# Optimization experiments

Measured on AMD Instinct MI355X. Metric: run time of the kernel, lower is better.

Reference implementation:

```python
import jax, jax.numpy as jnp
import numpy as np

B, N, E, H = 2, 2048, 2048, 16
D = E // H  # head_dim = 128


def setup_inputs() -> dict:
    key = jax.random.key(0)
    k1, k2, k3, k4 = jax.random.split(key, 4)
    x = jax.random.normal(k1, (B, N, E), dtype=jnp.float32)
    Wq = jax.random.normal(k2, (E, E), dtype=jnp.float32) * 0.02
    Wkv = jax.random.normal(k3, (2 * E, E), dtype=jnp.float32) * 0.02
    Wout = jax.random.normal(k4, (E, E), dtype=jnp.float32) * 0.02
    return {"x": x, "Wq": Wq, "Wkv": Wkv, "Wout": Wout}


def reference(x, Wq, Wkv, Wout):
    # projections (torch Linear: y = x @ W.T)
    q = x @ Wq.T                      # [b, n, e]
    kv = x @ Wkv.T                    # [b, n, 2e]
    k, v = jnp.split(kv, 2, axis=-1)  # each [b, n, e]

    def split_heads(t):
        return t.reshape(B, N, H, D).transpose(0, 2, 1, 3)  # [b, h, n, d]

    q, k, v = split_heads(q), split_heads(k), split_heads(v)

    scale = D ** -0.5
    sim = jnp.einsum('bhid,bhjd->bhij', q * scale, k)  # [b, h, n, n]

    # causal mask: triu(j - i + 1) masks strictly-future positions
    mask_value = -jnp.finfo(sim.dtype).max
    causal_mask = jnp.triu(jnp.ones((N, N), dtype=bool), k=1)
    sim = jnp.where(causal_mask, mask_value, sim)

    attn = jax.nn.softmax(sim, axis=-1)
    out = jnp.einsum('bhij,bhjd->bhid', attn, v)  # [b, h, n, d]
    out = out.transpose(0, 2, 1, 3).reshape(B, N, E)
    return out @ Wout.T
```

## Files before the change

### kernel.cpp

```cpp
#include <hip/hip_runtime.h>


typedef __bf16 bf16;
typedef bf16 bf16x2 __attribute__((ext_vector_type(2)));
typedef bf16 bf16x4 __attribute__((ext_vector_type(4)));
typedef bf16 bf16x8 __attribute__((ext_vector_type(8)));
typedef float f32x4 __attribute__((ext_vector_type(4)));
typedef float f32x16 __attribute__((ext_vector_type(16)));

typedef const __attribute__((address_space(1))) void cg_void;
typedef __attribute__((address_space(3))) void lds_void;

#define MFMA16(a, b, c) __builtin_amdgcn_mfma_f32_16x16x32_bf16((a), (b), (c), 0, 0, 0)
#define MFMA32(a, b, c) __builtin_amdgcn_mfma_f32_32x32x16_bf16((a), (b), (c), 0, 0, 0)

__device__ __forceinline__ void async_load16(const bf16* g, bf16* l) {
  __builtin_amdgcn_global_load_lds((cg_void*)g, (lds_void*)l, 16, 0, 0);
}

__global__ __launch_bounds__(256) void cast_all_kernel(
    const float* __restrict__ x, const float* __restrict__ wq,
    const float* __restrict__ wkv, const float* __restrict__ wout,
    bf16* __restrict__ xb, bf16* __restrict__ wqkvb, bf16* __restrict__ woutb) {
  long i = (long)blockIdx.x * 256 + threadIdx.x;
  const float* src; bf16* dst; long off;
  if (i < 1048576)      { src = x;    dst = xb;            off = i; }
  else if (i < 2621440) { src = wq;   dst = wqkvb;         off = i - 1048576;
                          if (off >= 524288) { src = wkv; dst = wqkvb + 4194304; off -= 524288; } }
  else                  { src = wout; dst = woutb;         off = i - 2621440; }
  float4 f0 = ((const float4*)src)[2 * off];
  float4 f1 = ((const float4*)src)[2 * off + 1];
  bf16x8 o;
  o[0] = (bf16)f0.x; o[1] = (bf16)f0.y; o[2] = (bf16)f0.z; o[3] = (bf16)f0.w;
  o[4] = (bf16)f1.x; o[5] = (bf16)f1.y; o[6] = (bf16)f1.z; o[7] = (bf16)f1.w;
  ((bf16x8*)dst)[off] = o;
}

#define STAGE_A(bufi, h, tt) do {                              \
    const bf16* g_ = Ag + (h) * 262144 + (tt) * 64;            \
    bf16* d_ = ldsA + (bufi) * 16384 + (h) * 8192;             \
    async_load16(g_, d_);                                      \
    async_load16(g_ + 131072, d_ + 4096);                      \
  } while (0)
#define STAGE_B(bufi, h, tt) do {                              \
    const bf16* g_ = Bg + (h) * 262144 + (tt) * 64;            \
    bf16* d_ = ldsB + (bufi) * 16384 + (h) * 8192;             \
    async_load16(g_, d_);                                      \
    async_load16(g_ + 131072, d_ + 4096);                      \
  } while (0)

__global__ __launch_bounds__(512, 2)
void gemm_qkv_8phase(const bf16* __restrict__ A, const bf16* __restrict__ B,
                     bf16* __restrict__ qk, bf16* __restrict__ vt) {
  __shared__ __attribute__((aligned(16))) bf16 sm[2][2][256][64];
  const int tid = threadIdx.x;
  const int lane = tid & 63;
  const int wid = tid >> 6;
  const int quad = lane >> 4, l15 = lane & 15;
  const int wr = wid >> 2, wc = wid & 3;

  const int lb = (blockIdx.x & 7) * 48 + (blockIdx.x >> 3);
  const int bn = lb % 24, bm = lb / 24;
  const int m0 = bm * 256, n0 = bn * 256;

  const int srow = tid >> 3;
  const int kswz8 = ((tid & 7) ^ (srow & 7)) * 8;
  const bf16* Ag = A + (size_t)(m0 + srow) * 2048 + kswz8;
  const bf16* Bg = B + (size_t)(n0 + srow) * 2048 + kswz8;
  bf16* ldsA = &sm[0][0][0][0] + tid * 8;
  bf16* ldsB = &sm[1][0][0][0] + tid * 8;

  f32x4 acc[8][4];
#pragma unroll
  for (int i = 0; i < 8; ++i)
#pragma unroll
    for (int j = 0; j < 4; ++j) acc[i][j] = {0.f, 0.f, 0.f, 0.f};

  const int r7 = l15 & 7;
  const int c0 = (quad ^ r7) * 8;
  const int c1 = ((4 + quad) ^ r7) * 8;
  const int arow = (wr * 128 + l15) * 64;
  const int brow = (wc * 64 + l15) * 64;

  STAGE_A(0, 0, 0); STAGE_A(0, 1, 0); STAGE_B(0, 0, 0); STAGE_B(0, 1, 0);
  STAGE_A(1, 0, 1);
  asm volatile("s_waitcnt vmcnt(2)" ::: "memory");
  __builtin_amdgcn_s_barrier();

  for (int t = 0; t < 32; ++t) {
    const int cur = t & 1;
    const bf16* as = &sm[0][0][0][0] + cur * 16384;
    const bf16* bs = &sm[1][0][0][0] + cur * 16384;
#pragma unroll
    for (int q = 0; q < 4; ++q) {
      const int fi = (q >> 1) * 4, fj = (q & 1) * 2;
      bf16x8 af[4][2], bfr[2][2];
#pragma unroll
      for (int i = 0; i < 4; ++i) {
        af[i][0] = *(const bf16x8*)(as + arow + (fi + i) * 1024 + c0);
        af[i][1] = *(const bf16x8*)(as + arow + (fi + i) * 1024 + c1);
      }
#pragma unroll
      for (int j = 0; j < 2; ++j) {
        bfr[j][0] = *(const bf16x8*)(bs + brow + (fj + j) * 1024 + c0);
        bfr[j][1] = *(const bf16x8*)(bs + brow + (fj + j) * 1024 + c1);
      }
      if (t < 31) {
        const int nb = 1 - cur;
        if (q == 0) STAGE_A(nb, 1, t + 1);
        if (q == 1) STAGE_B(nb, 0, t + 1);
        if (q == 2) STAGE_B(nb, 1, t + 1);
      }
      __builtin_amdgcn_s_barrier();
      asm volatile("s_waitcnt lgkmcnt(0)" ::: "memory");
      __builtin_amdgcn_s_setprio(1);
#pragma unroll
      for (int ks = 0; ks < 2; ++ks)
#pragma unroll
        for (int i = 0; i < 4; ++i)
#pragma unroll
          for (int j = 0; j < 2; ++j)
            acc[fi + i][fj + j] = MFMA16(af[i][ks], bfr[j][ks], acc[fi + i][fj + j]);
      __builtin_amdgcn_s_setprio(0);
      __builtin_amdgcn_s_barrier();
    }
    if (t < 30) {
      STAGE_A(cur, 0, t + 2);
      asm volatile("s_waitcnt vmcnt(2)" ::: "memory");
      __builtin_amdgcn_s_barrier();
    } else if (t == 30) {
      asm volatile("s_waitcnt vmcnt(0)" ::: "memory");
      __builtin_amdgcn_s_barrier();
    }
  }

  if (n0 < 4096) {
#pragma unroll
    for (int i = 0; i < 8; ++i)
#pragma unroll
      for (int r = 0; r < 4; ++r) {
        const size_t base = (size_t)(m0 + wr * 128 + i * 16 + quad * 4 + r) * 4096
                          + n0 + wc * 64 + l15;
#pragma unroll
        for (int j = 0; j < 4; ++j) qk[base + j * 16] = (bf16)acc[i][j][r];
      }
  } else {
    __syncthreads();
    bf16* T = &sm[0][0][0][0];
#pragma unroll
    for (int i = 0; i < 8; ++i)
#pragma unroll
      for (int r = 0; r < 4; ++r) {
        const int nl = wr * 128 + i * 16 + quad * 4 + r;
#pragma unroll
        for (int j = 0; j < 4; ++j) {
          const int fl = wc * 64 + j * 16 + l15;
          T[fl * 256 + ((((nl >> 3) ^ (fl & 31)) << 3) | (nl & 7))] = (bf16)acc[i][j][r];
        }
      }
    __syncthreads();
    const int f0g = n0 - 4096, nb0 = m0 & 2047, b = m0 >> 11;
#pragma unroll
    for (int c = 0; c < 16; ++c) {
      const int idx = c * 512 + tid;
      const int fl = idx >> 5, nb = idx & 31;
      bf16x8 o = *(const bf16x8*)(T + fl * 256 + ((nb ^ (fl & 31)) << 3));
      *(bf16x8*)(vt + (size_t)(b * 2048 + f0g + fl) * 2048 + nb0 + nb * 8) = o;
    }
  }
}

__global__ __launch_bounds__(256, 4)
void gemm_out_kernel(const bf16* __restrict__ A, const bf16* __restrict__ B,
                     float* __restrict__ C, int K, int NN) {
  __shared__ __attribute__((aligned(16))) bf16 smem[8192];
  bf16* As = smem;
  bf16* Bs = smem + 4096;
  const int tid = threadIdx.x;
  const int wave = tid >> 6, lane = tid & 63;
  const int quad = lane >> 4, l15 = lane & 15;
  const int m0 = blockIdx.y * 128, n0 = blockIdx.x * 128;
  const int wm = (wave >> 1) * 64, wn = (wave & 1) * 64;

  f32x4 acc[4][4];
#pragma unroll
  for (int i = 0; i < 4; ++i)
#pragma unroll
    for (int j = 0; j < 4; ++j) acc[i][j] = {0.f, 0.f, 0.f, 0.f};

  const int srow = tid >> 2;
  const int scol = (tid & 3) * 8;
  const bf16* aG = A + (size_t)(m0 + srow) * K + scol;
  const bf16* bG = B + (size_t)(n0 + srow) * K + scol;
  bf16* aL = As + srow * 32 + scol;
  bf16* bL = Bs + srow * 32 + scol;
  const size_t gstep = (size_t)64 * K;

  for (int kt = 0; kt < K; kt += 32) {
    __syncthreads();
    async_load16(aG, aL);
    async_load16(aG + gstep, aL + 64 * 32);
    async_load16(bG, bL);
    async_load16(bG + gstep, bL + 64 * 32);
    aG += 32; bG += 32;
    __syncthreads();

    bf16x8 af[4], bfr[4];
#pragma unroll
    for (int i = 0; i < 4; ++i)
      af[i] = *(const bf16x8*)(As + (wm + i * 16 + l15) * 32 + quad * 8);
#pragma unroll
    for (int j = 0; j < 4; ++j)
      bfr[j] = *(const bf16x8*)(Bs + (wn + j * 16 + l15) * 32 + quad * 8);
#pragma unroll
    for (int i = 0; i < 4; ++i)
#pragma unroll
      for (int j = 0; j < 4; ++j) acc[i][j] = MFMA16(af[i], bfr[j], acc[i][j]);
  }

#pragma unroll
  for (int i = 0; i < 4; ++i) {
#pragma unroll
    for (int r = 0; r < 4; ++r) {
      int row = m0 + wm + i * 16 + quad * 4 + r;
      size_t base = (size_t)row * NN + n0 + wn + l15;
#pragma unroll
      for (int j = 0; j < 4; ++j) C[base + j * 16] = (float)acc[i][j][r];
    }
  }
}

__global__ __launch_bounds__(256, 2)
void attn_kernel(const bf16* __restrict__ qk, const bf16* __restrict__ vt,
                 bf16* __restrict__ yb) {
  constexpr int NSEQ = 2048, E = 2048, QKS = 4096;
  __shared__ __attribute__((aligned(16))) bf16 Ks[2][64 * 128];
  __shared__ __attribute__((aligned(16))) bf16 Vs[2][128 * 64];
  const int tid = threadIdx.x;
  const int wave = tid >> 6, lane = tid & 63;
  const int l31 = lane & 31, half = lane >> 5;
  const int id = blockIdx.x;
  const int slot = (id >> 5) & 15;
  const int bh = (id & 7) | (((id >> 3) & 3) << 3);
  const int b = bh >> 4, h = bh & 15;
  const int qt = (slot < 8) ? slot : 23 - slot;
  const float c1 = 0.08838834764831845f * 1.44269504088896f;

  const int krow_s = tid >> 4, kch_s = tid & 15;
  const int vrow_s = tid >> 3, vch_s = tid & 7;
  const bf16* kg = qk + (size_t)(b * NSEQ) * QKS + 2048 + h * 128;
  const bf16* vg = vt + (size_t)b * E * NSEQ + (size_t)(h * 128) * NSEQ;

  const int diag = 2 * qt + (wave >> 1);
  const int ktmax = 2 * qt + 1;

  {
    bf16* kdst = Ks[0] + tid * 8;
    bf16* vdst = Vs[0] + tid * 8;
#pragma unroll
    for (int p = 0; p < 4; ++p) {
      int r = p * 16 + krow_s;
      async_load16(kg + (size_t)r * QKS + (kch_s ^ (r & 7)) * 8, kdst + p * 2048);
    }
#pragma unroll
    for (int p = 0; p < 4; ++p) {
      int r = p * 32 + vrow_s;
      async_load16(vg + (size_t)r * NSEQ + (vch_s ^ (r & 7)) * 8, vdst + p * 2048);
    }
  }

  const int qrow = qt * 128 + wave * 32 + l31;
  bf16x8 qf[8];
  {
    const bf16* qp = qk + (size_t)(b * NSEQ + qrow) * QKS + h * 128 + half * 8;
#pragma unroll
    for (int k8 = 0; k8 < 8; ++k8) qf[k8] = *(const bf16x8*)(qp + k8 * 16);
  }

  float m = -3.0e38f, l = 0.f;
  f32x16 accO[4];
#pragma unroll
  for (int md = 0; md < 4; ++md)
#pragma unroll
    for (int r = 0; r < 16; ++r) accO[md][r] = 0.f;

  union PU { unsigned u; bf16x2 h; };
  union FU { bf16x8 v; unsigned u[4]; };

  for (int kt = 0; kt <= ktmax; ++kt) {
    const int cur = kt & 1;
    __syncthreads();

    if (kt < ktmax) {
      const int nxt = kt + 1;
      bf16* kdst = Ks[1 - cur] + tid * 8;
      bf16* vdst = Vs[1 - cur] + tid * 8;
#pragma unroll
      for (int p = 0; p < 4; ++p) {
        int r = p * 16 + krow_s;
        async_load16(kg + (size_t)(nxt * 64 + r) * QKS + (kch_s ^ (r & 7)) * 8, kdst + p * 2048);
      }
#pragma unroll
      for (int p = 0; p < 4; ++p) {
        int r = p * 32 + vrow_s;
        async_load16(vg + (size_t)r * NSEQ + nxt * 64 + (vch_s ^ (r & 7)) * 8, vdst + p * 2048);
      }
    }

    if (kt > diag) continue;

    const bf16* ks = Ks[cur];
    const bf16* vs = Vs[cur];

    f32x16 st[2];
#pragma unroll
    for (int mt = 0; mt < 2; ++mt)
#pragma unroll
      for (int r = 0; r < 16; ++r) st[mt][r] = 0.f;
#pragma unroll
    for (int k8 = 0; k8 < 8; ++k8) {
#pragma unroll
      for (int mt = 0; mt < 2; ++mt) {
        int row = mt * 32 + l31;
        int sl = (k8 * 2 + half) ^ (row & 7);
        bf16x8 kf = *(const bf16x8*)(ks + row * 128 + sl * 8);
        st[mt] = MFMA32(kf, qf[k8], st[mt]);
      }
    }

    if (kt == diag) {
#pragma unroll
      for (int mt = 0; mt < 2; ++mt)
#pragma unroll
        for (int r = 0; r < 16; ++r) {
          int t = kt * 64 + mt * 32 + (r & 3) + 8 * (r >> 2) + 4 * half;
          if (t > qrow) st[mt][r] = -3.0e38f;
        }
    }

    float mx = -3.0e38f;
#pragma unroll
    for (int mt = 0; mt < 2; ++mt)
#pragma unroll
      for (int r = 0; r < 16; ++r) mx = fmaxf(mx, st[mt][r]);
    mx = fmaxf(mx, __shfl_xor(mx, 32));
    float mnew = fmaxf(m, mx);
    float alpha = exp2f((m - mnew) * c1);
    float mc = mnew * c1;
    m = mnew;

    float psum = 0.f;
    unsigned pown[2][4][2];
#pragma unroll
    for (int mt = 0; mt < 2; ++mt)
#pragma unroll
      for (int qd = 0; qd < 4; ++qd)
#pragma unroll
        for (int pr = 0; pr < 2; ++pr) {
          float p0 = exp2f(st[mt][qd * 4 + pr * 2] * c1 - mc);
          float p1 = exp2f(st[mt][qd * 4 + pr * 2 + 1] * c1 - mc);
          psum += p0 + p1;
          PU a; a.h[0] = (bf16)p0; a.h[1] = (bf16)p1;
          pown[mt][qd][pr] = a.u;
        }
    psum += __shfl_xor(psum, 32);
    l = l * alpha + psum;

#pragma unroll
    for (int md = 0; md < 4; ++md)
#pragma unroll
      for (int r = 0; r < 16; ++r) accO[md][r] *= alpha;

#pragma unroll
    for (int mt = 0; mt < 2; ++mt)
#pragma unroll
      for (int c = 0; c < 2; ++c) {
        const int qa = 2 * c, qb = 2 * c + 1;
        unsigned ra0 = __shfl_xor(pown[mt][qa][0], 32);
        unsigned ra1 = __shfl_xor(pown[mt][qa][1], 32);
        unsigned rb0 = __shfl_xor(pown[mt][qb][0], 32);
        unsigned rb1 = __shfl_xor(pown[mt][qb][1], 32);
        FU f;
        f.u[0] = half ? rb0 : pown[mt][qa][0];
        f.u[1] = half ? rb1 : pown[mt][qa][1];
        f.u[2] = half ? pown[mt][qb][0] : ra0;
        f.u[3] = half ? pown[mt][qb][1] : ra1;
        const int kk = mt * 2 + c;
#pragma unroll
        for (int md = 0; md < 4; ++md) {
          int row = md * 32 + l31;
          bf16x8 vf = *(const bf16x8*)(vs + row * 64 + (((kk * 2 + half) ^ (row & 7)) * 8));
          accO[md] = MFMA32(vf, f.v, accO[md]);
        }
      }
  }

  float invl = 1.0f / l;
  bf16* yp = yb + (size_t)(b * NSEQ + qrow) * E + h * 128;
#pragma unroll
  for (int md = 0; md < 4; ++md)
#pragma unroll
    for (int rq = 0; rq < 4; ++rq) {
      bf16x4 o;
#pragma unroll
      for (int i = 0; i < 4; ++i) o[i] = (bf16)(accO[md][rq * 4 + i] * invl);
      *(bf16x4*)(yp + md * 32 + rq * 8 + half * 4) = o;
    }
}

extern "C" void kernel_launch(void* const* d_in, const int* in_sizes, int n_in,
                              void* d_out, int out_size, void* d_ws, size_t ws_size,
                              hipStream_t stream) {
  const float* x    = (const float*)d_in[0];
  const float* Wq   = (const float*)d_in[1];
  const float* Wkv  = (const float*)d_in[2];
  const float* Wout = (const float*)d_in[3];
  float* out = (float*)d_out;

  constexpr size_t NX = (size_t)2 * 2048 * 2048;
  constexpr size_t NW = (size_t)2048 * 2048;

  bf16* xb     = (bf16*)d_ws;
  bf16* wqkvb  = xb + NX;
  bf16* woutb  = wqkvb + 3 * NW;
  bf16* qk_b   = woutb + NW;
  bf16* y_b    = qk_b + 2 * NX;
  bf16* vt_b   = y_b + NX;

  cast_all_kernel<<<12288, 256, 0, stream>>>(x, Wq, Wkv, Wout, xb, wqkvb, woutb);

  gemm_qkv_8phase<<<384, 512, 0, stream>>>(xb, wqkvb, qk_b, vt_b);
  attn_kernel<<<512, 256, 0, stream>>>(qk_b, vt_b, y_b);
  gemm_out_kernel<<<dim3(16, 32), 256, 0, stream>>>(y_b, woutb, out, 2048, 2048);
}
```

Before: 388.2 us.

## Restructure QKV GEMM inner loop to k-step phases and prefetch A two tiles ahead

The main loop of the QKV projection GEMM now runs two k-step phases per tile instead of four output-quadrant phases. Each phase loads all 8 A fragments and 4 B fragments and issues 32 MFMAs, which halves the barriers per tile and lengthens each MFMA burst. Both A halves are now staged two tiles ahead and B is staged one tile ahead per phase, which changes the vmcnt waits. The cost is more live fragment registers, which could reduce occupancy or cause spills.

```diff
diff --git a/kernel.cpp b/kernel.cpp
--- a/kernel.cpp
+++ b/kernel.cpp
@@ -77,14 +77,12 @@
     for (int j = 0; j < 4; ++j) acc[i][j] = {0.f, 0.f, 0.f, 0.f};
 
   const int r7 = l15 & 7;
-  const int c0 = (quad ^ r7) * 8;
-  const int c1 = ((4 + quad) ^ r7) * 8;
   const int arow = (wr * 128 + l15) * 64;
   const int brow = (wc * 64 + l15) * 64;
 
   STAGE_A(0, 0, 0); STAGE_A(0, 1, 0); STAGE_B(0, 0, 0); STAGE_B(0, 1, 0);
-  STAGE_A(1, 0, 1);
-  asm volatile("s_waitcnt vmcnt(2)" ::: "memory");
+  STAGE_A(1, 0, 1); STAGE_A(1, 1, 1);
+  asm volatile("s_waitcnt vmcnt(4)" ::: "memory");
   __builtin_amdgcn_s_barrier();
 
   for (int t = 0; t < 32; ++t) {
@@ -92,41 +90,29 @@
     const bf16* as = &sm[0][0][0][0] + cur * 16384;
     const bf16* bs = &sm[1][0][0][0] + cur * 16384;
 #pragma unroll
-    for (int q = 0; q < 4; ++q) {
-      const int fi = (q >> 1) * 4, fj = (q & 1) * 2;
-      bf16x8 af[4][2], bfr[2][2];
-#pragma unroll
-      for (int i = 0; i < 4; ++i) {
-        af[i][0] = *(const bf16x8*)(as + arow + (fi + i) * 1024 + c0);
-        af[i][1] = *(const bf16x8*)(as + arow + (fi + i) * 1024 + c1);
-      }
-#pragma unroll
-      for (int j = 0; j < 2; ++j) {
-        bfr[j][0] = *(const bf16x8*)(bs + brow + (fj + j) * 1024 + c0);
-        bfr[j][1] = *(const bf16x8*)(bs + brow + (fj + j) * 1024 + c1);
-      }
-      if (t < 31) {
-        const int nb = 1 - cur;
-        if (q == 0) STAGE_A(nb, 1, t + 1);
-        if (q == 1) STAGE_B(nb, 0, t + 1);
-        if (q == 2) STAGE_B(nb, 1, t + 1);
-      }
+    for (int ks = 0; ks < 2; ++ks) {
+      const int cc = ((ks * 4 + quad) ^ r7) * 8;
+      bf16x8 af[8], bfr[4];
+#pragma unroll
+      for (int i = 0; i < 8; ++i)
+        af[i] = *(const bf16x8*)(as + arow + i * 1024 + cc);
+#pragma unroll
+      for (int j = 0; j < 4; ++j)
+        bfr[j] = *(const bf16x8*)(bs + brow + j * 1024 + cc);
+      if (t < 31) STAGE_B(1 - cur, ks, t + 1);
       __builtin_amdgcn_s_barrier();
       asm volatile("s_waitcnt lgkmcnt(0)" ::: "memory");
       __builtin_amdgcn_s_setprio(1);
 #pragma unroll
-      for (int ks = 0; ks < 2; ++ks)
-#pragma unroll
-        for (int i = 0; i < 4; ++i)
-#pragma unroll
-          for (int j = 0; j < 2; ++j)
-            acc[fi + i][fj + j] = MFMA16(af[i][ks], bfr[j][ks], acc[fi + i][fj + j]);
+      for (int i = 0; i < 8; ++i)
+#pragma unroll
+        for (int j = 0; j < 4; ++j) acc[i][j] = MFMA16(af[i], bfr[j], acc[i][j]);
       __builtin_amdgcn_s_setprio(0);
       __builtin_amdgcn_s_barrier();
     }
     if (t < 30) {
-      STAGE_A(cur, 0, t + 2);
-      asm volatile("s_waitcnt vmcnt(2)" ::: "memory");
+      STAGE_A(cur, 0, t + 2); STAGE_A(cur, 1, t + 2);
+      asm volatile("s_waitcnt vmcnt(4)" ::: "memory");
       __builtin_amdgcn_s_barrier();
     } else if (t == 30) {
       asm volatile("s_waitcnt vmcnt(0)" ::: "memory");
```

New measurement: 366.6 us. -5.5%, faster.
